# Optimization experiments

Measured on AMD Instinct MI355X. Metric: run time of the kernel, lower is better.

The kernel has to match this reference:

```python
import jax, jax.numpy as jnp
import numpy as np

TR = 14.7e-3
NT = 144
TAU = 1.8
T0 = TAU
T1B = 1.65
FA_PARAMS = (3.0, 12.0)
B = 262144


def _build_buffers():
    # t = arange(Nt)*TR + t0
    t = np.arange(NT, dtype=np.float64) * TR + T0
    # QUADRATIC flip-angle schedule: all t >= t0, so N = Nt
    n = NT
    alpha = FA_PARAMS[0] + (FA_PARAMS[1] - FA_PARAMS[0]) * (np.arange(n) / (n - 1)) ** 2
    # Attenuation recursion: R[0]=1, R[i]=R[i-1]*cos(deg2rad(alpha[i-1])) for t[i]>t0
    R = np.concatenate([[1.0], np.cumprod(np.cos(np.deg2rad(alpha[:-1])))])
    return (t.astype(np.float32), alpha.astype(np.float32), R.astype(np.float32))


def setup_inputs() -> dict:
    key = jax.random.key(0)
    x = jax.random.uniform(key, (B, 4), dtype=jnp.float32)  # [delta_t, s, p, amp]
    t, alpha, R = _build_buffers()
    return {"x": x, "t": jnp.asarray(t), "alpha": jnp.asarray(alpha), "R": jnp.asarray(R)}


def _togammainc(X, A):
    # scipy clamps negatives to 0 in both args, then regularized lower incomplete gamma P(A, X)
    X = jnp.maximum(X, 0.0)
    A = jnp.broadcast_to(jnp.maximum(A, 0.0), X.shape)
    return jax.scipy.special.gammainc(A, X)


def reference(x, t, alpha, R):
    delta_t = x[:, 0:1]  # [B,1]
    s = x[:, 1:2]
    p = x[:, 2:3]
    amp = x[:, 3:4]

    a = 1.0 + p * s                     # [B,1]
    sprime = s + 1.0 / T1B              # [B,1]
    SF = 2.0 * jnp.exp(-delta_t / T1B) * (s / sprime) ** a  # [B,1]

    td = t[None, :] - delta_t           # [B,Nt]
    G = _togammainc(sprime * td, a) - _togammainc(sprime * (td - TAU), a)  # [B,Nt]
    E = jnp.sin(jnp.deg2rad(alpha))     # [Nt]

    S = SF * R[None, :] * G * E[None, :]  # [B,Nt]
    return amp * S
```

## Files before the change

kernel.cpp:

```cpp
#include <hip/hip_runtime.h>
#include <cmath>

#define NT 144

typedef float v2f __attribute__((ext_vector_type(2)));


__global__ __launch_bounds__(256) void dynangio_kernel(
    const float* __restrict__ x,
    const float* __restrict__ t,
    const float* __restrict__ alpha,
    const float* __restrict__ R,
    float* __restrict__ out,
    int B)
{
    __shared__ alignas(16) float sh_t[NT];
    __shared__ alignas(16) float sh_re[NT];
    const int tid = threadIdx.x;
    if (tid < NT) {
        float al = alpha[tid];
        sh_t[tid]  = t[tid];
        sh_re[tid] = R[tid] * sinf(al * 0.017453292519943295f);
    }
    __syncthreads();

    const int i = blockIdx.x * blockDim.x + tid;
    if (i >= B) return;

    const float4 xi = reinterpret_cast<const float4*>(x)[i];
    const float dt  = xi.x;
    const float s   = xi.y;
    const float p   = xi.z;
    const float amp = xi.w;

    const float T1B   = 1.65f;
    const float TAU   = 1.8f;
    const float LOG2E = 1.4426950408889634f;

    const float u  = p * s;
    const float a  = 1.0f + u;
    const float sp = s + (1.0f / T1B);

    float g = 0.035868343f;
    g = g * u - 0.193527818f;
    g = g * u + 0.482199394f;
    g = g * u - 0.756704078f;
    g = g * u + 0.918206857f;
    g = g * u - 0.897056937f;
    g = g * u + 0.988205891f;
    g = g * u - 0.577191652f;
    g = g * u + 1.0f;
    const float Ga1 = (1.0f + u) * g;

    const float d18 = a + 18.0f;
    const float d17 = (a + 17.0f) * d18;
    const float d16 = (a + 16.0f) * d17;
    const float d15 = (a + 15.0f) * d16;
    const float d14 = (a + 14.0f) * d15;
    const float d13 = (a + 13.0f) * d14;
    const float d12 = (a + 12.0f) * d13;
    const float d11 = (a + 11.0f) * d12;
    const float d10 = (a + 10.0f) * d11;
    const float d9  = (a +  9.0f) * d10;
    const float d8  = (a +  8.0f) * d9;
    const float d7  = (a +  7.0f) * d8;
    const float d6  = (a +  6.0f) * d7;
    const float d5  = (a +  5.0f) * d6;
    const float d4  = (a +  4.0f) * d5;
    const float d3  = (a +  3.0f) * d4;
    const float d2  = (a +  2.0f) * d3;
    const float d1  = (a +  1.0f) * d2;

    const float invDG = 1.0f / (d1 * Ga1);

    const float SF = 2.0f * __builtin_amdgcn_exp2f(
        a * (__builtin_amdgcn_logf(s) - __builtin_amdgcn_logf(sp))
        - dt * (LOG2E / T1B));

    const float crow  = amp * SF * invDG;
    const float nspdt = -sp * dt;
    const float spTau = sp * TAU;

    auto elem = [&](float tj, float rej) -> float {
        const float x1 = __builtin_fmaf(sp, tj, nspdt);
        const float x2 = fmaxf(x1 - spTau, 0.0f);
        v2f X; X.x = x1; X.y = x2;
        v2f N = {1.0f, 1.0f};
        N = X * N + d18;  N = X * N + d17;  N = X * N + d16;
        N = X * N + d15;  N = X * N + d14;  N = X * N + d13;
        N = X * N + d12;  N = X * N + d11;  N = X * N + d10;
        N = X * N + d9;   N = X * N + d8;   N = X * N + d7;
        N = X * N + d6;   N = X * N + d5;   N = X * N + d4;
        N = X * N + d3;   N = X * N + d2;   N = X * N + d1;
        v2f L; L.x = __builtin_amdgcn_logf(x1); L.y = __builtin_amdgcn_logf(x2);
        v2f Ee = a * L - X * LOG2E;
        const float e1 = __builtin_amdgcn_exp2f(Ee.x);
        const float e2 = __builtin_amdgcn_exp2f(Ee.y);
        const float gg = __builtin_fmaf(N.x, e1, -(N.y * e2));
        return (crow * rej) * gg;
    };

    float* __restrict__ orow = out + (size_t)i * NT;
    const float4* sh_t4  = reinterpret_cast<const float4*>(sh_t);
    const float4* sh_re4 = reinterpret_cast<const float4*>(sh_re);

    #pragma unroll 2
    for (int jb = 0; jb < NT / 4; ++jb) {
        const float4 tj4 = sh_t4[jb];
        const float4 re4 = sh_re4[jb];
        float4 res;
        res.x = elem(tj4.x, re4.x);
        res.y = elem(tj4.y, re4.y);
        res.z = elem(tj4.z, re4.z);
        res.w = elem(tj4.w, re4.w);
        reinterpret_cast<float4*>(orow)[jb] = res;
    }
}

extern "C" void kernel_launch(void* const* d_in, const int* in_sizes, int n_in,
                              void* d_out, int out_size, void* d_ws, size_t ws_size,
                              hipStream_t stream) {
    const float* x     = (const float*)d_in[0];
    const float* t     = (const float*)d_in[1];
    const float* alpha = (const float*)d_in[2];
    const float* R     = (const float*)d_in[3];
    float* out = (float*)d_out;

    const int B = in_sizes[0] / 4;
    const int threads = 256;
    const int blocks = (B + threads - 1) / threads;
    hipLaunchKernelGGL(dynangio_kernel, dim3(blocks), dim3(threads), 0, stream,
                       x, t, alpha, R, out, B);
}
```

Before: 196.3 us.

## Split each row across four threads to coalesce output stores

```diff
diff --git a/kernel.cpp b/kernel.cpp
--- a/kernel.cpp
+++ b/kernel.cpp
@@ -18,16 +18,16 @@
     __shared__ alignas(16) float sh_re[NT];
     const int tid = threadIdx.x;
     if (tid < NT) {
-        float al = alpha[tid];
         sh_t[tid]  = t[tid];
-        sh_re[tid] = R[tid] * sinf(al * 0.017453292519943295f);
+        sh_re[tid] = R[tid] * sinf(alpha[tid] * 0.017453292519943295f);
     }
     __syncthreads();
 
-    const int i = blockIdx.x * blockDim.x + tid;
-    if (i >= B) return;
+    const int c   = tid & 3;
+    const int row = blockIdx.x * 64 + (tid >> 2);
+    if (row >= B) return;
 
-    const float4 xi = reinterpret_cast<const float4*>(x)[i];
+    const float4 xi = reinterpret_cast<const float4*>(x)[row];
     const float dt  = xi.x;
     const float s   = xi.y;
     const float p   = xi.z;
@@ -86,12 +86,12 @@
         const float x2 = fmaxf(x1 - spTau, 0.0f);
         v2f X; X.x = x1; X.y = x2;
         v2f N = {1.0f, 1.0f};
-        N = X * N + d18;  N = X * N + d17;  N = X * N + d16;
-        N = X * N + d15;  N = X * N + d14;  N = X * N + d13;
-        N = X * N + d12;  N = X * N + d11;  N = X * N + d10;
-        N = X * N + d9;   N = X * N + d8;   N = X * N + d7;
-        N = X * N + d6;   N = X * N + d5;   N = X * N + d4;
-        N = X * N + d3;   N = X * N + d2;   N = X * N + d1;
+        N = X*N + d18;  N = X*N + d17;  N = X*N + d16;
+        N = X*N + d15;  N = X*N + d14;  N = X*N + d13;
+        N = X*N + d12;  N = X*N + d11;  N = X*N + d10;
+        N = X*N + d9;   N = X*N + d8;   N = X*N + d7;
+        N = X*N + d6;   N = X*N + d5;   N = X*N + d4;
+        N = X*N + d3;   N = X*N + d2;   N = X*N + d1;
         v2f L; L.x = __builtin_amdgcn_logf(x1); L.y = __builtin_amdgcn_logf(x2);
         v2f Ee = a * L - X * LOG2E;
         const float e1 = __builtin_amdgcn_exp2f(Ee.x);
@@ -100,20 +100,21 @@
         return (crow * rej) * gg;
     };
 
-    float* __restrict__ orow = out + (size_t)i * NT;
+    float4* __restrict__ orow4 = reinterpret_cast<float4*>(out + (size_t)row * NT);
     const float4* sh_t4  = reinterpret_cast<const float4*>(sh_t);
     const float4* sh_re4 = reinterpret_cast<const float4*>(sh_re);
 
-    #pragma unroll 2
-    for (int jb = 0; jb < NT / 4; ++jb) {
-        const float4 tj4 = sh_t4[jb];
-        const float4 re4 = sh_re4[jb];
+    #pragma unroll 3
+    for (int k = 0; k < 9; ++k) {
+        const int ch = c + 4 * k;
+        const float4 tj4 = sh_t4[ch];
+        const float4 re4 = sh_re4[ch];
         float4 res;
         res.x = elem(tj4.x, re4.x);
         res.y = elem(tj4.y, re4.y);
         res.z = elem(tj4.z, re4.z);
         res.w = elem(tj4.w, re4.w);
-        reinterpret_cast<float4*>(orow)[jb] = res;
+        orow4[ch] = res;
     }
 }
 
@@ -127,8 +128,8 @@
     float* out = (float*)d_out;
 
     const int B = in_sizes[0] / 4;
-    const int threads = 256;
-    const int blocks = (B + threads - 1) / threads;
-    hipLaunchKernelGGL(dynangio_kernel, dim3(blocks), dim3(threads), 0, stream,
+    const int rows_per_block = 64;
+    const int blocks = (B + rows_per_block - 1) / rows_per_block;
+    hipLaunchKernelGGL(dynangio_kernel, dim3(blocks), dim3(256), 0, stream,
                        x, t, alpha, R, out, B);
 }
```

Result: faster. 173.7 us (-11.5%).
